# Kernel optimization log

Hardware: AMD Instinct MI355X
Metric: run time of the kernel (lower is better)

Reference implementation:

```python
import jax, jax.numpy as jnp
import numpy as np

K = 256
Q = 64
T = 500001  # length of return series r


def setup_inputs() -> dict:
    key = jax.random.key(0)
    k_r, k_b, k_w0, k_w = jax.random.split(key, 4)
    r = 0.01 * jax.random.normal(k_r, (T,), dtype=jnp.float32)
    a0 = jnp.float32(0.0)
    a1 = jnp.float32(0.0)
    raw_beta0 = jnp.float32(-4.0)
    raw_beta = (-4.0 + 0.1 * jax.random.normal(k_b, (K,))).astype(jnp.float32)
    raw_w0 = (-8.0 + 0.1 * jax.random.normal(k_w0, (K,))).astype(jnp.float32)
    raw_w = (-4.0 + 0.1 * jax.random.normal(k_w, (K, Q))).astype(jnp.float32)
    return {"r": r, "a0": a0, "a1": a1, "raw_beta0": raw_beta0,
            "raw_beta": raw_beta, "raw_w0": raw_w0, "raw_w": raw_w}


def reference(r, a0, a1, raw_beta0, raw_beta, raw_w0, raw_w):
    # AR(1) residuals
    u = r[1:] - a0 - a1 * r[:-1]          # [T-1]
    u2 = u * u                            # [T-1]
    n = u.shape[0]
    # init_u2 = unbiased variance of u2, repeated q times (torch.var default ddof=1)
    init_u2 = jnp.full((Q,), jnp.var(u2, ddof=1), dtype=u2.dtype)
    u2_full = jnp.concatenate([init_u2, u2])  # [q + T-1]
    # vectorized windowing: row t holds u2_full[t+q-1], ..., u2_full[t] (flipped window)
    t_idx = jnp.arange(n)[:, None]        # [n,1]
    lag_idx = jnp.arange(Q)[None, :]      # [1,q]
    idx = (Q + t_idx) - 1 - lag_idx       # [n,q]
    u2_lags = u2_full[idx]                # [n,q]
    # softplus-MLP volatility
    w0 = jax.nn.softplus(raw_w0)          # [k]
    w = jax.nn.softplus(raw_w)            # [k,q]
    h = jax.nn.relu(w0[None, :] + u2_lags @ w.T)  # [n,k]
    beta0 = jax.nn.softplus(raw_beta0)
    beta = jax.nn.softplus(raw_beta)      # [k]
    sigma2 = beta0 + h @ beta + 1e-8      # [n]
    # Gaussian negative log-likelihood
    nll = (0.5 * n * jnp.log(jnp.float32(2.0 * np.pi))
           + 0.5 * jnp.sum(jnp.log(sigma2))
           + 0.5 * jnp.sum(u2 / sigma2))
    return nll
```

## Files before the change

kernel.cpp:

```cpp
#include <hip/hip_runtime.h>
#include <math.h>

#define K_ 256
#define Q_ 64
#define NT 500000
#define NTILES (NT / 16)
#define TT_ 16
#define NBLK ((NT + 255) / 256)
#define GRID_MAIN ((NTILES + TT_ - 1) / TT_)

#define WS_BETA0  2
#define WS_U2     4
#define WS_U2B0   (WS_U2 + Q_ + NT)
#define WS_U2B1   (WS_U2B0 + (Q_ + NT + 1) / 2)
#define WS_BPACK  (WS_U2B1 + (Q_ + NT + 1) / 2)
#define WS_W0     (WS_BPACK + 8192)
#define WS_BETA   (WS_W0 + K_)
#define WS_PART   (WS_BETA + K_)
#define WS_PART2  (WS_PART + 2048)
#define WS_OUT    (WS_PART2 + 2048)

typedef __attribute__((ext_vector_type(8))) __bf16 bf16x8;
typedef __attribute__((ext_vector_type(4))) float  f32x4;

__device__ __forceinline__ float softplusf(float x) {
    return (x > 20.f) ? x : log1pf(__expf(x));
}

__device__ __forceinline__ unsigned short f2bf(float f) {
    unsigned int u = __float_as_uint(f);
    u = u + 0x7FFFu + ((u >> 16) & 1u);
    return (unsigned short)(u >> 16);
}

__global__ void k_u2(const float* __restrict__ r,
                     const float* __restrict__ a0p,
                     const float* __restrict__ a1p,
                     float* __restrict__ ws) {
    __shared__ float red[8];
    int i = blockIdx.x * blockDim.x + threadIdx.x;
    float a0 = a0p[0], a1 = a1p[0];
    float v = 0.f, v2 = 0.f;
    if (i < NT) {
        float u  = r[i + 1] - a0 - a1 * r[i];
        float u2 = u * u;
        ws[WS_U2 + Q_ + i] = u2;
        unsigned short b = f2bf(u2);
        ((unsigned short*)(ws + WS_U2B0))[Q_ + i]     = b;
        ((unsigned short*)(ws + WS_U2B1))[Q_ + i - 1] = b;
        v = u2; v2 = u2 * u2;
    }
    #pragma unroll
    for (int off = 32; off > 0; off >>= 1) {
        v  += __shfl_down(v,  off, 64);
        v2 += __shfl_down(v2, off, 64);
    }
    int wv = threadIdx.x >> 6;
    if ((threadIdx.x & 63) == 0) { red[wv * 2] = v; red[wv * 2 + 1] = v2; }
    __syncthreads();
    if (threadIdx.x == 0) {
        ws[WS_PART  + blockIdx.x] = red[0] + red[2] + red[4] + red[6];
        ws[WS_PART2 + blockIdx.x] = red[1] + red[3] + red[5] + red[7];
    }
}

__global__ void k_prep(const float* __restrict__ raw_beta0,
                       const float* __restrict__ raw_beta,
                       const float* __restrict__ raw_w0,
                       const float* __restrict__ raw_w,
                       float* __restrict__ ws) {
    int idx = blockIdx.x * blockDim.x + threadIdx.x;
    if (idx < 16384) {
        int jj = idx & 7, l = (idx >> 3) & 63, s = (idx >> 9) & 1, kc = idx >> 10;
        int j    = 32 * s + 8 * (l >> 4) + jj;
        int kout = kc * 16 + (l & 15);
        ((unsigned short*)(ws + WS_BPACK))[idx] =
            f2bf(softplusf(raw_w[kout * Q_ + (Q_ - 1 - j)]));
    } else if (idx < 16384 + K_) {
        int k = idx - 16384;
        ws[WS_W0 + k] = softplusf(raw_w0[k]);
    } else if (idx < 16384 + 2 * K_) {
        int k = idx - (16384 + K_);
        ws[WS_BETA + k] = softplusf(raw_beta[k]);
    } else if (idx < 16384 + 2 * K_ + Q_) {
        int j = idx - (16384 + 2 * K_);
        float s1 = 0.f, s2 = 0.f;
        for (int p = j; p < NBLK; p += 64) {
            s1 += ws[WS_PART  + p];
            s2 += ws[WS_PART2 + p];
        }
        #pragma unroll
        for (int mask = 1; mask < 64; mask <<= 1) {
            s1 += __shfl_xor(s1, mask, 64);
            s2 += __shfl_xor(s2, mask, 64);
        }
        float n  = (float)NT;
        float var = (s2 - s1 * s1 / n) / (n - 1.f);
        unsigned short b = f2bf(var);
        ((unsigned short*)(ws + WS_U2B0))[j] = b;
        if (j < Q_ - 1) ((unsigned short*)(ws + WS_U2B1))[j] = b;
        if (j == 0) ws[WS_BETA0] = softplusf(raw_beta0[0]);
    }
}

__launch_bounds__(256, 4)
__global__ void k_main(float* __restrict__ ws) {
    __shared__ __align__(16) float sig[TT_ * 256];
    __shared__ float red[4];

    int tid = threadIdx.x;
    int l = tid & 63, w = tid >> 6;
    int m = l & 15, q = l >> 4;

    const unsigned short* bp = (const unsigned short*)(ws + WS_BPACK);
    const float* u2f = ws + WS_U2;
    float beta0v = ws[WS_BETA0];

    bf16x8 Wf[4][2];
    f32x4 w0c[4], betc[4];
    #pragma unroll
    for (int i = 0; i < 4; ++i) {
        int kc = w * 4 + i;
        #pragma unroll
        for (int s = 0; s < 2; ++s)
            __builtin_memcpy(&Wf[i][s], bp + ((kc * 2 + s) * 64 + l) * 8, 16);
        w0c[i] = *(const f32x4*)(ws + WS_W0   + kc * 16 + q * 4);
        betc[i] = *(const f32x4*)(ws + WS_BETA + kc * 16 + q * 4);
    }

    int par = m & 1;
    const char* abase = (const char*)(ws + (par ? WS_U2B1 : WS_U2B0));
    int tile0 = blockIdx.x * TT_;
    int aoff = (tile0 * 16 + m + 8 * q - par) * 2;

    bf16x8 U0, U1, U0n, U1n;
    __builtin_memcpy(&U0, abase + aoff, 16);
    __builtin_memcpy(&U1, abase + aoff + 64, 16);

    #pragma unroll 2
    for (int it = 0; it < TT_; ++it) {
        int anext = aoff + 32;
        __builtin_memcpy(&U0n, abase + anext, 16);
        __builtin_memcpy(&U1n, abase + anext + 64, 16);

        float p[4];
        #pragma unroll
        for (int i = 0; i < 4; ++i) {
            f32x4 acc = __builtin_amdgcn_mfma_f32_16x16x32_bf16(Wf[i][0], U0, w0c[i], 0, 0, 0);
            acc = __builtin_amdgcn_mfma_f32_16x16x32_bf16(Wf[i][1], U1, acc, 0, 0, 0);
            float pi;
            pi = betc[i][0] * fmaxf(acc[0], 0.f);
            pi = fmaf(betc[i][1], fmaxf(acc[1], 0.f), pi);
            pi = fmaf(betc[i][2], fmaxf(acc[2], 0.f), pi);
            pi = fmaf(betc[i][3], fmaxf(acc[3], 0.f), pi);
            p[i] = pi;
        }
        sig[it * 256 + tid] = (p[0] + p[1]) + (p[2] + p[3]);

        aoff = anext; U0 = U0n; U1 = U1n;
    }

    __syncthreads();

    int tile = tid >> 4, tt = tid & 15;
    const float* sp = &sig[tile * 256 + tt];
    float s = 0.f;
    #pragma unroll
    for (int wq = 0; wq < 16; ++wq) s += sp[wq * 16];
    float sg = beta0v + s + 1e-8f;
    int t = tile0 * 16 + tid;
    float val = (t < NT) ? (__logf(sg) + u2f[Q_ + t] / sg) : 0.f;

    #pragma unroll
    for (int mask = 1; mask < 64; mask <<= 1)
        val += __shfl_xor(val, mask, 64);
    if (l == 0) red[w] = val;
    __syncthreads();
    if (tid == 0)
        ws[WS_OUT + blockIdx.x] = red[0] + red[1] + red[2] + red[3];
}

__global__ void k_final(const float* __restrict__ ws, float* __restrict__ out) {
    __shared__ float red[4];
    int tid = threadIdx.x;
    float s = 0.f;
    for (int p = tid; p < GRID_MAIN; p += 256) s += ws[WS_OUT + p];
    #pragma unroll
    for (int mask = 1; mask < 64; mask <<= 1)
        s += __shfl_xor(s, mask, 64);
    if ((tid & 63) == 0) red[tid >> 6] = s;
    __syncthreads();
    if (tid == 0)
        out[0] = 0.5f * (float)NT * 1.8378770664093453f
               + 0.5f * (red[0] + red[1] + red[2] + red[3]);
}

extern "C" void kernel_launch(void* const* d_in, const int* in_sizes, int n_in,
                              void* d_out, int out_size, void* d_ws, size_t ws_size,
                              hipStream_t stream) {
    const float* r        = (const float*)d_in[0];
    const float* a0       = (const float*)d_in[1];
    const float* a1       = (const float*)d_in[2];
    const float* raw_b0   = (const float*)d_in[3];
    const float* raw_beta = (const float*)d_in[4];
    const float* raw_w0   = (const float*)d_in[5];
    const float* raw_w    = (const float*)d_in[6];
    float* out = (float*)d_out;
    float* ws  = (float*)d_ws;

    k_u2<<<NBLK, 256, 0, stream>>>(r, a0, a1, ws);

    int prep_threads = 16384 + 2 * K_ + Q_;
    k_prep<<<(prep_threads + 255) / 256, 256, 0, stream>>>(
        raw_b0, raw_beta, raw_w0, raw_w, ws);

    k_main<<<GRID_MAIN, 256, 0, stream>>>(ws);

    k_final<<<1, 256, 0, stream>>>(ws, out);
}
```

Before: 102.7 us.

## Fuse prep into one front kernel and fold final reduction into main

Merges the residual/bf16 pass and the weight softplus packing into a single launch. The variance finalization moves into block 0 of the main kernel, and the final sum moves into the main kernel through a last-block atomic counter, so four launches become two. The main kernel now recomputes u^2 from r instead of reading a stored fp32 u2 array, removing that write and read. It also pads the shared sig buffer to a stride of 272 to reduce LDS bank conflicts. In exchange it adds an atomic, thread fences and a small serial tail in the last block, and it relies on only block 0 reading the initial-variance lag values.

```diff
diff --git a/kernel.cpp b/kernel.cpp
--- a/kernel.cpp
+++ b/kernel.cpp
@@ -8,10 +8,12 @@
 #define TT_ 16
 #define NBLK ((NT + 255) / 256)
 #define GRID_MAIN ((NTILES + TT_ - 1) / TT_)
-
+#define PREP_THREADS (16384 + 2 * K_)
+#define PREP_BLOCKS ((PREP_THREADS + 255) / 256)
+
+#define WS_CNT    0
 #define WS_BETA0  2
-#define WS_U2     4
-#define WS_U2B0   (WS_U2 + Q_ + NT)
+#define WS_U2B0   4
 #define WS_U2B1   (WS_U2B0 + (Q_ + NT + 1) / 2)
 #define WS_BPACK  (WS_U2B1 + (Q_ + NT + 1) / 2)
 #define WS_W0     (WS_BPACK + 8192)
@@ -33,88 +35,100 @@
     return (unsigned short)(u >> 16);
 }
 
-__global__ void k_u2(const float* __restrict__ r,
-                     const float* __restrict__ a0p,
-                     const float* __restrict__ a1p,
-                     float* __restrict__ ws) {
+__global__ void k_front(const float* __restrict__ r,
+                        const float* __restrict__ a0p,
+                        const float* __restrict__ a1p,
+                        const float* __restrict__ raw_beta0,
+                        const float* __restrict__ raw_beta,
+                        const float* __restrict__ raw_w0,
+                        const float* __restrict__ raw_w,
+                        float* __restrict__ ws) {
     __shared__ float red[8];
-    int i = blockIdx.x * blockDim.x + threadIdx.x;
-    float a0 = a0p[0], a1 = a1p[0];
-    float v = 0.f, v2 = 0.f;
-    if (i < NT) {
-        float u  = r[i + 1] - a0 - a1 * r[i];
-        float u2 = u * u;
-        ws[WS_U2 + Q_ + i] = u2;
-        unsigned short b = f2bf(u2);
-        ((unsigned short*)(ws + WS_U2B0))[Q_ + i]     = b;
-        ((unsigned short*)(ws + WS_U2B1))[Q_ + i - 1] = b;
-        v = u2; v2 = u2 * u2;
-    }
-    #pragma unroll
-    for (int off = 32; off > 0; off >>= 1) {
-        v  += __shfl_down(v,  off, 64);
-        v2 += __shfl_down(v2, off, 64);
-    }
-    int wv = threadIdx.x >> 6;
-    if ((threadIdx.x & 63) == 0) { red[wv * 2] = v; red[wv * 2 + 1] = v2; }
-    __syncthreads();
-    if (threadIdx.x == 0) {
-        ws[WS_PART  + blockIdx.x] = red[0] + red[2] + red[4] + red[6];
-        ws[WS_PART2 + blockIdx.x] = red[1] + red[3] + red[5] + red[7];
-    }
-}
-
-__global__ void k_prep(const float* __restrict__ raw_beta0,
-                       const float* __restrict__ raw_beta,
-                       const float* __restrict__ raw_w0,
-                       const float* __restrict__ raw_w,
-                       float* __restrict__ ws) {
-    int idx = blockIdx.x * blockDim.x + threadIdx.x;
-    if (idx < 16384) {
-        int jj = idx & 7, l = (idx >> 3) & 63, s = (idx >> 9) & 1, kc = idx >> 10;
-        int j    = 32 * s + 8 * (l >> 4) + jj;
-        int kout = kc * 16 + (l & 15);
-        ((unsigned short*)(ws + WS_BPACK))[idx] =
-            f2bf(softplusf(raw_w[kout * Q_ + (Q_ - 1 - j)]));
-    } else if (idx < 16384 + K_) {
-        int k = idx - 16384;
-        ws[WS_W0 + k] = softplusf(raw_w0[k]);
-    } else if (idx < 16384 + 2 * K_) {
-        int k = idx - (16384 + K_);
-        ws[WS_BETA + k] = softplusf(raw_beta[k]);
-    } else if (idx < 16384 + 2 * K_ + Q_) {
-        int j = idx - (16384 + 2 * K_);
-        float s1 = 0.f, s2 = 0.f;
-        for (int p = j; p < NBLK; p += 64) {
-            s1 += ws[WS_PART  + p];
-            s2 += ws[WS_PART2 + p];
-        }
-        #pragma unroll
-        for (int mask = 1; mask < 64; mask <<= 1) {
-            s1 += __shfl_xor(s1, mask, 64);
-            s2 += __shfl_xor(s2, mask, 64);
-        }
-        float n  = (float)NT;
-        float var = (s2 - s1 * s1 / n) / (n - 1.f);
-        unsigned short b = f2bf(var);
-        ((unsigned short*)(ws + WS_U2B0))[j] = b;
-        if (j < Q_ - 1) ((unsigned short*)(ws + WS_U2B1))[j] = b;
-        if (j == 0) ws[WS_BETA0] = softplusf(raw_beta0[0]);
+    int bi = blockIdx.x - NBLK;
+    if (bi < 0) {
+        int i = blockIdx.x * blockDim.x + threadIdx.x;
+        float a0 = a0p[0], a1 = a1p[0];
+        float v = 0.f, v2 = 0.f;
+        if (i < NT) {
+            float u  = r[i + 1] - a0 - a1 * r[i];
+            float u2 = u * u;
+            unsigned short b = f2bf(u2);
+            ((unsigned short*)(ws + WS_U2B0))[Q_ + i]     = b;
+            ((unsigned short*)(ws + WS_U2B1))[Q_ + i - 1] = b;
+            v = u2; v2 = u2 * u2;
+        }
+        #pragma unroll
+        for (int off = 32; off > 0; off >>= 1) {
+            v  += __shfl_down(v,  off, 64);
+            v2 += __shfl_down(v2, off, 64);
+        }
+        int wv = threadIdx.x >> 6;
+        if ((threadIdx.x & 63) == 0) { red[wv * 2] = v; red[wv * 2 + 1] = v2; }
+        __syncthreads();
+        if (threadIdx.x == 0) {
+            ws[WS_PART  + blockIdx.x] = red[0] + red[2] + red[4] + red[6];
+            ws[WS_PART2 + blockIdx.x] = red[1] + red[3] + red[5] + red[7];
+        }
+    } else {
+        int idx = bi * 256 + threadIdx.x;
+        if (idx < 16384) {
+            int jj = idx & 7, l = (idx >> 3) & 63, s = (idx >> 9) & 1, kc = idx >> 10;
+            int j    = 32 * s + 8 * (l >> 4) + jj;
+            int kout = kc * 16 + (l & 15);
+            ((unsigned short*)(ws + WS_BPACK))[idx] =
+                f2bf(softplusf(raw_w[kout * Q_ + (Q_ - 1 - j)]));
+        } else if (idx < 16384 + K_) {
+            int k = idx - 16384;
+            ws[WS_W0 + k] = softplusf(raw_w0[k]);
+            if (k == 0) {
+                ws[WS_BETA0] = softplusf(raw_beta0[0]);
+                ((unsigned int*)ws)[WS_CNT] = 0u;
+            }
+        } else if (idx < 16384 + 2 * K_) {
+            int k = idx - (16384 + K_);
+            ws[WS_BETA + k] = softplusf(raw_beta[k]);
+        }
     }
 }
 
 __launch_bounds__(256, 4)
-__global__ void k_main(float* __restrict__ ws) {
-    __shared__ __align__(16) float sig[TT_ * 256];
+__global__ void k_main(const float* __restrict__ r,
+                       const float* __restrict__ a0p,
+                       const float* __restrict__ a1p,
+                       float* __restrict__ ws,
+                       float* __restrict__ out) {
+    __shared__ __align__(16) float sig[TT_ * 272];
     __shared__ float red[4];
+    __shared__ int amLast;
 
     int tid = threadIdx.x;
     int l = tid & 63, w = tid >> 6;
     int m = l & 15, q = l >> 4;
 
+    if (blockIdx.x == 0) {
+        if (tid < 64) {
+            float s1 = 0.f, s2 = 0.f;
+            for (int p = tid; p < NBLK; p += 64) {
+                s1 += ws[WS_PART  + p];
+                s2 += ws[WS_PART2 + p];
+            }
+            #pragma unroll
+            for (int mask = 1; mask < 64; mask <<= 1) {
+                s1 += __shfl_xor(s1, mask, 64);
+                s2 += __shfl_xor(s2, mask, 64);
+            }
+            float n   = (float)NT;
+            float var = (s2 - s1 * s1 / n) / (n - 1.f);
+            unsigned short b = f2bf(var);
+            ((unsigned short*)(ws + WS_U2B0))[tid] = b;
+            if (tid < Q_ - 1) ((unsigned short*)(ws + WS_U2B1))[tid] = b;
+        }
+        __syncthreads();
+    }
+
     const unsigned short* bp = (const unsigned short*)(ws + WS_BPACK);
-    const float* u2f = ws + WS_U2;
     float beta0v = ws[WS_BETA0];
+    float a0 = a0p[0], a1 = a1p[0];
 
     bf16x8 Wf[4][2];
     f32x4 w0c[4], betc[4];
@@ -124,7 +138,7 @@
         #pragma unroll
         for (int s = 0; s < 2; ++s)
             __builtin_memcpy(&Wf[i][s], bp + ((kc * 2 + s) * 64 + l) * 8, 16);
-        w0c[i] = *(const f32x4*)(ws + WS_W0   + kc * 16 + q * 4);
+        w0c[i]  = *(const f32x4*)(ws + WS_W0   + kc * 16 + q * 4);
         betc[i] = *(const f32x4*)(ws + WS_BETA + kc * 16 + q * 4);
     }
 
@@ -155,7 +169,7 @@
             pi = fmaf(betc[i][3], fmaxf(acc[3], 0.f), pi);
             p[i] = pi;
         }
-        sig[it * 256 + tid] = (p[0] + p[1]) + (p[2] + p[3]);
+        sig[it * 272 + tid] = (p[0] + p[1]) + (p[2] + p[3]);
 
         aoff = anext; U0 = U0n; U1 = U1n;
     }
@@ -163,13 +177,17 @@
     __syncthreads();
 
     int tile = tid >> 4, tt = tid & 15;
-    const float* sp = &sig[tile * 256 + tt];
+    const float* sp = &sig[tile * 272 + tt];
     float s = 0.f;
     #pragma unroll
     for (int wq = 0; wq < 16; ++wq) s += sp[wq * 16];
     float sg = beta0v + s + 1e-8f;
     int t = tile0 * 16 + tid;
-    float val = (t < NT) ? (__logf(sg) + u2f[Q_ + t] / sg) : 0.f;
+    float val = 0.f;
+    if (t < NT) {
+        float u = r[t + 1] - a0 - a1 * r[t];
+        val = __logf(sg) + u * u / sg;
+    }
 
     #pragma unroll
     for (int mask = 1; mask < 64; mask <<= 1)
@@ -178,21 +196,26 @@
     __syncthreads();
     if (tid == 0)
         ws[WS_OUT + blockIdx.x] = red[0] + red[1] + red[2] + red[3];
-}
-
-__global__ void k_final(const float* __restrict__ ws, float* __restrict__ out) {
-    __shared__ float red[4];
-    int tid = threadIdx.x;
-    float s = 0.f;
-    for (int p = tid; p < GRID_MAIN; p += 256) s += ws[WS_OUT + p];
-    #pragma unroll
-    for (int mask = 1; mask < 64; mask <<= 1)
-        s += __shfl_xor(s, mask, 64);
-    if ((tid & 63) == 0) red[tid >> 6] = s;
+
+    __threadfence();
+    if (tid == 0) {
+        unsigned c = atomicAdd((unsigned int*)ws + WS_CNT, 1u);
+        amLast = (c == GRID_MAIN - 1);
+    }
     __syncthreads();
-    if (tid == 0)
-        out[0] = 0.5f * (float)NT * 1.8378770664093453f
-               + 0.5f * (red[0] + red[1] + red[2] + red[3]);
+    if (amLast) {
+        __threadfence();
+        float fs = 0.f;
+        for (int p = tid; p < GRID_MAIN; p += 256) fs += ws[WS_OUT + p];
+        #pragma unroll
+        for (int mask = 1; mask < 64; mask <<= 1)
+            fs += __shfl_xor(fs, mask, 64);
+        if (l == 0) red[w] = fs;
+        __syncthreads();
+        if (tid == 0)
+            out[0] = 0.5f * (float)NT * 1.8378770664093453f
+                   + 0.5f * (red[0] + red[1] + red[2] + red[3]);
+    }
 }
 
 extern "C" void kernel_launch(void* const* d_in, const int* in_sizes, int n_in,
@@ -208,13 +231,8 @@
     float* out = (float*)d_out;
     float* ws  = (float*)d_ws;
 
-    k_u2<<<NBLK, 256, 0, stream>>>(r, a0, a1, ws);
-
-    int prep_threads = 16384 + 2 * K_ + Q_;
-    k_prep<<<(prep_threads + 255) / 256, 256, 0, stream>>>(
-        raw_b0, raw_beta, raw_w0, raw_w, ws);
-
-    k_main<<<GRID_MAIN, 256, 0, stream>>>(ws);
-
-    k_final<<<1, 256, 0, stream>>>(ws, out);
-}
+    k_front<<<NBLK + PREP_BLOCKS, 256, 0, stream>>>(
+        r, a0, a1, raw_b0, raw_beta, raw_w0, raw_w, ws);
+
+    k_main<<<GRID_MAIN, 256, 0, stream>>>(r, a0, a1, ws, out);
+}
```

Result: slower. 230.6 us (+124.6%).
